# Optimization experiments

Measured on AMD Instinct MI355X. Metric: run time of the kernel, lower is better.

Reference implementation:

```python
import jax, jax.numpy as jnp
import numpy as np

B, N, D, K = 2, 8192, 512, 16


def setup_inputs() -> dict:
    key = jax.random.key(0)
    k1, k2, k3, k4 = jax.random.split(key, 4)
    x = jax.random.normal(k1, (B, N, D), dtype=jnp.float32)
    xyz = jax.random.normal(k2, (B, N, 3), dtype=jnp.float32)
    # nn.Linear(d_model, 3*d_model): weight [3D, D], bias [3D]
    W_qkv = jax.random.normal(k3, (3 * D, D), dtype=jnp.float32) * 0.02
    b_qkv = jnp.zeros((3 * D,), dtype=jnp.float32)
    # nn.Linear(d_model, d_model)
    W_fc = jax.random.normal(k4, (D, D), dtype=jnp.float32) * 0.02
    b_fc = jnp.zeros((D,), dtype=jnp.float32)
    return {"x": x, "xyz": xyz, "W_qkv": W_qkv, "b_qkv": b_qkv, "W_fc": W_fc, "b_fc": b_fc}


def _knn_idx(xyz):
    # squared-distance KNN (same ordering as cdist): |a|^2 + |b|^2 - 2 a.b
    sq = jnp.sum(xyz * xyz, axis=-1)                      # [B, N]
    d2 = sq[:, :, None] + sq[:, None, :] - 2.0 * jnp.einsum('bnc,bmc->bnm', xyz, xyz)
    return jax.lax.top_k(-d2, K)[1]                       # [B, N, K] smallest distances


def reference(x, xyz, W_qkv, b_qkv, W_fc, b_fc):
    knn_idx = _knn_idx(xyz)                               # no-grad in original
    qkv = jnp.einsum('bnd,ed->bne', x, W_qkv) + b_qkv     # [B, N, 3D]
    qkv = qkv.reshape(B, N, 3, D)
    q, k, v = qkv[:, :, 0], qkv[:, :, 1], qkv[:, :, 2]    # [B, N, D]
    gather = jax.vmap(lambda arr, idx: arr[idx])          # per-batch neighbor gather
    k_neigh = gather(k, knn_idx)                          # [B, N, K, D]
    v_neigh = gather(v, knn_idx)                          # [B, N, K, D]
    # faithful to einsum('bnd,bnsk->bns', q, k_neigh): sums d and feature dims independently
    attn = (q.sum(-1)[:, :, None] * k_neigh.sum(-1)) / jnp.sqrt(jnp.float32(D))  # [B, N, K]
    attn = jax.nn.softmax(attn, axis=2)[..., None]        # [B, N, K, 1]
    x_out = (attn * v_neigh).sum(axis=2)                  # [B, N, D]
    return jnp.einsum('bnd,ed->bne', x_out, W_fc) + b_fc + x
```

## Files before the change

kernel.cpp:

```cpp
#include <hip/hip_runtime.h>

typedef _Float16 half_t;
typedef _Float16 half8 __attribute__((ext_vector_type(8)));
typedef _Float16 half4v __attribute__((ext_vector_type(4)));
typedef float f32x4 __attribute__((ext_vector_type(4)));
typedef float f32x2 __attribute__((ext_vector_type(2)));

#define NB 2
#define NN 8192
#define ND 512
#define NKNN 16
#define BN (NB*NN)

#define OFF_XH   0ull
#define OFF_VH   (OFF_XH  + (size_t)BN*ND*2)
#define OFF_XOH  (OFF_VH  + (size_t)BN*ND*2)
#define OFF_WVH  (OFF_XOH + (size_t)BN*ND*2)
#define OFF_WFCH (OFF_WVH + (size_t)ND*ND*2)
#define OFF_XW   (OFF_WFCH+ (size_t)ND*ND*2)
#define OFF_XW2  (OFF_XW  + (size_t)BN*16)
#define OFF_IDX  (OFF_XW2 + (size_t)BN*16)
#define OFF_WQC  (OFF_IDX + (size_t)BN*NKNN*4)
#define OFF_WKC  (OFF_WQC + 2048)
#define OFF_QKB  (OFF_WKC + 2048)
#define OFF_QS   (OFF_QKB + 256)
#define OFF_KS   (OFF_QS  + (size_t)BN*4)

__global__ __launch_bounds__(256) void kcolsum(const float* __restrict__ W,
                                               float* __restrict__ wq,
                                               float* __restrict__ wk) {
  int h = blockIdx.x >> 3, g = blockIdx.x & 7;
  int t = threadIdx.x, dl = t & 63, s = t >> 6;
  const float* Wb = W + (size_t)h * 512 * 512;
  int d = g * 64 + dl;
  float acc = 0.f;
  for (int e = s * 128; e < s * 128 + 128; ++e) acc += Wb[(size_t)e * 512 + d];
  __shared__ float red[4][64];
  red[s][dl] = acc;
  __syncthreads();
  if (s == 0) (h ? wk : wq)[d] = red[0][dl] + red[1][dl] + red[2][dl] + red[3][dl];
}

__global__ __launch_bounds__(512) void kbias(const float* __restrict__ b,
                                             float* __restrict__ qkb) {
  __shared__ float r0[512], r1[512];
  int t = threadIdx.x;
  r0[t] = b[t]; r1[t] = b[512 + t];
  __syncthreads();
  for (int s = 256; s; s >>= 1) {
    if (t < s) { r0[t] += r0[t + s]; r1[t] += r1[t + s]; }
    __syncthreads();
  }
  if (t == 0) { qkb[0] = r0[0]; qkb[1] = r1[0]; }
}

__global__ __launch_bounds__(256) void kconvw(const float* __restrict__ wqkv,
                                              const float* __restrict__ wfc,
                                              half_t* __restrict__ wvh,
                                              half_t* __restrict__ wfch) {
  int i = blockIdx.x * 256 + threadIdx.x;
  float4 a = ((const float4*)(wqkv + 1024 * 512))[i];
  half4v ha; ha[0]=(half_t)a.x; ha[1]=(half_t)a.y; ha[2]=(half_t)a.z; ha[3]=(half_t)a.w;
  *(half4v*)(wvh + (size_t)i * 4) = ha;
  float4 c = ((const float4*)wfc)[i];
  half4v hc; hc[0]=(half_t)c.x; hc[1]=(half_t)c.y; hc[2]=(half_t)c.z; hc[3]=(half_t)c.w;
  *(half4v*)(wfch + (size_t)i * 4) = hc;
}

__global__ __launch_bounds__(256) void kxh(const float* __restrict__ x,
                                           const float* __restrict__ wq,
                                           const float* __restrict__ wk,
                                           const float* __restrict__ qkb,
                                           half_t* __restrict__ xh,
                                           float* __restrict__ qs,
                                           float* __restrict__ ks) {
  int wid = blockIdx.x * 4 + (threadIdx.x >> 6);
  int l = threadIdx.x & 63;
  size_t base = (size_t)wid * ND + l * 8;
  float4 a0 = *(const float4*)(x + base);
  float4 a1 = *(const float4*)(x + base + 4);
  half8 h;
  h[0]=(half_t)a0.x; h[1]=(half_t)a0.y; h[2]=(half_t)a0.z; h[3]=(half_t)a0.w;
  h[4]=(half_t)a1.x; h[5]=(half_t)a1.y; h[6]=(half_t)a1.z; h[7]=(half_t)a1.w;
  *(half8*)(xh + base) = h;
  float4 q0 = ((const float4*)(wq + l * 8))[0], q1 = ((const float4*)(wq + l * 8))[1];
  float4 k0 = ((const float4*)(wk + l * 8))[0], k1 = ((const float4*)(wk + l * 8))[1];
  float dq = a0.x*q0.x + a0.y*q0.y + a0.z*q0.z + a0.w*q0.w
           + a1.x*q1.x + a1.y*q1.y + a1.z*q1.z + a1.w*q1.w;
  float dk = a0.x*k0.x + a0.y*k0.y + a0.z*k0.z + a0.w*k0.w
           + a1.x*k1.x + a1.y*k1.y + a1.z*k1.z + a1.w*k1.w;
  #pragma unroll
  for (int o = 32; o; o >>= 1) { dq += __shfl_xor(dq, o); dk += __shfl_xor(dk, o); }
  if (l == 0) { qs[wid] = dq + qkb[0]; ks[wid] = dk + qkb[1]; }
}

__global__ __launch_bounds__(256) void kxyzw(const float* __restrict__ xyz,
                                             float4* __restrict__ xw,
                                             float4* __restrict__ xw2) {
  int p = blockIdx.x * 256 + threadIdx.x;
  int b = p >> 12;
  int pl = p & 4095;
  int i0 = b * NN + pl * 2;
  const float* s = xyz + (size_t)i0 * 3;
  float x0 = s[0], y0 = s[1], z0 = s[2];
  float x1 = s[3], y1 = s[4], z1 = s[5];
  float sq0 = __fadd_rn(__fadd_rn(__fmul_rn(x0, x0), __fmul_rn(y0, y0)), __fmul_rn(z0, z0));
  float sq1 = __fadd_rn(__fadd_rn(__fmul_rn(x1, x1), __fmul_rn(y1, y1)), __fmul_rn(z1, z1));
  xw[i0]     = make_float4(x0, y0, z0, sq0);
  xw[i0 + 1] = make_float4(x1, y1, z1, sq1);
  xw2[(size_t)b * NN + pl]          = make_float4(x0, x1, y0, y1);
  xw2[(size_t)b * NN + NN/2 + pl]   = make_float4(z0, z1, sq0, sq1);
}

#define QPW 4
__global__ __launch_bounds__(256, 4) void kknn(const float4* __restrict__ xw,
                                               const float4* __restrict__ xw2,
                                               int* __restrict__ idxo) {
  __shared__ __align__(16) float4 tile[1024];
  const int tid = threadIdx.x;
  const int l = tid & 63;
  const int w = tid >> 6;
  const int b = blockIdx.x >> 9;
  const int qbase = (blockIdx.x & 511) * (4 * QPW) + w * QPW;
  const float4* xb  = xw  + (size_t)b * NN;
  const float4* xa2 = xw2 + (size_t)b * NN;
  const float4* xb2 = xa2 + NN / 2;

  f32x2 qxx[QPW], qyy[QPW], qzz[QPW], qww[QPW];
  #pragma unroll
  for (int qi = 0; qi < QPW; ++qi) {
    float4 qp = xb[qbase + qi];
    qxx[qi] = (f32x2){qp.x, qp.x};
    qyy[qi] = (f32x2){qp.y, qp.y};
    qzz[qi] = (f32x2){qp.z, qp.z};
    qww[qi] = (f32x2){qp.w, qp.w};
  }
  const f32x2 m2 = (f32x2){-2.0f, -2.0f};

  float mind[QPW]; int mini[QPW];
  #pragma unroll
  for (int qi = 0; qi < QPW; ++qi) { mind[qi] = __builtin_inff(); mini[qi] = 0x7fffffff; }

  for (int t = 0; t < 8; ++t) {
    __syncthreads();
    tile[tid]       = xa2[t * 512 + tid];
    tile[256 + tid] = xa2[t * 512 + 256 + tid];
    tile[512 + tid] = xb2[t * 512 + tid];
    tile[768 + tid] = xb2[t * 512 + 256 + tid];
    __syncthreads();
    #pragma unroll
    for (int it = 0; it < 8; ++it) {
      int p = it * 64 + l;
      float4 A = tile[p];
      float4 Bv = tile[512 + p];
      f32x2 cx = (f32x2){A.x, A.y};
      f32x2 cy = (f32x2){A.z, A.w};
      f32x2 cz = (f32x2){Bv.x, Bv.y};
      f32x2 cw = (f32x2){Bv.z, Bv.w};
      int ci0 = t * 1024 + p * 2;
      #pragma unroll
      for (int qi = 0; qi < QPW; ++qi) {
        f32x2 dot = __builtin_elementwise_fma(qzz[qi], cz,
                      __builtin_elementwise_fma(qyy[qi], cy, qxx[qi] * cx));
        f32x2 s2 = qww[qi] + cw;
        f32x2 d2 = __builtin_elementwise_fma(m2, dot, s2);
        if (d2.x < mind[qi]) { mind[qi] = d2.x; mini[qi] = ci0; }
        if (d2.y < mind[qi]) { mind[qi] = d2.y; mini[qi] = ci0 + 1; }
      }
    }
  }

  float kd[QPW]; int ki[QPW]; float wst[QPW];
  #pragma unroll
  for (int qi = 0; qi < QPW; ++qi) {
    float d = mind[qi]; int ii = mini[qi];
    #pragma unroll
    for (int k = 2; k <= 64; k <<= 1) {
      #pragma unroll
      for (int j = k >> 1; j > 0; j >>= 1) {
        float od = __shfl_xor(d, j);
        int   oi = __shfl_xor(ii, j);
        bool up = ((l & k) == 0);
        bool lower_lane = ((l & j) == 0);
        bool oless = (od < d) || (od == d && oi < ii);
        bool take = (up == lower_lane) ? oless : !oless;
        if (take) { d = od; ii = oi; }
      }
    }
    kd[qi] = __shfl(d, l & 15);
    ki[qi] = __shfl(ii, l & 15);
    wst[qi] = __shfl(d, 15);
  }

  auto insert = [&](bool ok, float dv, int iv, int qi) {
    unsigned long long m = __ballot(ok);
    while (m) {
      int a = __builtin_ctzll(m);
      m &= m - 1;
      float dc = __shfl(dv, a);
      int ic = __shfl(iv, a);
      bool lower = (kd[qi] < dc) || (kd[qi] == dc && ki[qi] < ic);
      int r = __popcll(__ballot(lower) & 0xFFFFull);
      if (r < 16) {
        float pd = __shfl_up(kd[qi], 1, 16);
        int pi = __shfl_up(ki[qi], 1, 16);
        int pp = l & 15;
        if (pp == r)      { kd[qi] = dc; ki[qi] = ic; }
        else if (pp > r)  { kd[qi] = pd; ki[qi] = pi; }
        wst[qi] = __shfl(kd[qi], 15, 16);
      }
    }
  };

  for (int t = 0; t < 8; ++t) {
    __syncthreads();
    tile[tid]       = xa2[t * 512 + tid];
    tile[256 + tid] = xa2[t * 512 + 256 + tid];
    tile[512 + tid] = xb2[t * 512 + tid];
    tile[768 + tid] = xb2[t * 512 + 256 + tid];
    __syncthreads();
    #pragma unroll 2
    for (int it = 0; it < 8; ++it) {
      int p = it * 64 + l;
      float4 A = tile[p];
      float4 Bv = tile[512 + p];
      f32x2 cx = (f32x2){A.x, A.y};
      f32x2 cy = (f32x2){A.z, A.w};
      f32x2 cz = (f32x2){Bv.x, Bv.y};
      f32x2 cw = (f32x2){Bv.z, Bv.w};
      int ci0 = t * 1024 + p * 2;
      #pragma unroll
      for (int qi = 0; qi < QPW; ++qi) {
        f32x2 dot = __builtin_elementwise_fma(qzz[qi], cz,
                      __builtin_elementwise_fma(qyy[qi], cy, qxx[qi] * cx));
        f32x2 s2 = qww[qi] + cw;
        f32x2 d2 = __builtin_elementwise_fma(m2, dot, s2);
        bool ok0 = (d2.x <= wst[qi]) && (ci0 != mini[qi]);
        bool ok1 = (d2.y <= wst[qi]) && (ci0 + 1 != mini[qi]);
        insert(ok0, d2.x, ci0, qi);
        insert(ok1, d2.y, ci0 + 1, qi);
      }
    }
  }

  if (l < 16) {
    #pragma unroll
    for (int qi = 0; qi < QPW; ++qi)
      idxo[((size_t)b * NN + qbase + qi) * NKNN + l] = ki[qi];
  }
}

__device__ __forceinline__ void gload16(const void* g, void* l) {
  __builtin_amdgcn_global_load_lds((const __attribute__((address_space(1))) void*)g,
                                   (__attribute__((address_space(3))) void*)l, 16, 0, 0);
}

template <int EPI>
__global__ __launch_bounds__(256) void kgemm(const half_t* __restrict__ A,
                                             const half_t* __restrict__ Bw,
                                             const float* __restrict__ bias,
                                             const float* __restrict__ resid,
                                             void* __restrict__ Cout) {
  __shared__ __align__(16) half_t As[128 * 64];
  __shared__ __align__(16) half_t Bs[128 * 64];
  const int tid = threadIdx.x;
  const int l = tid & 63;
  const int w = tid >> 6;
  const int wm = w >> 1, wn = w & 1;
  const int mt = blockIdx.x >> 2;
  const int nt = blockIdx.x & 3;
  const int lr = l & 15, lg = l >> 4;

  f32x4 acc[4][4];
  #pragma unroll
  for (int i = 0; i < 4; ++i)
    #pragma unroll
    for (int j = 0; j < 4; ++j) acc[i][j] = (f32x4){0.f, 0.f, 0.f, 0.f};

  for (int kt = 0; kt < 8; ++kt) {
    #pragma unroll
    for (int i = 0; i < 4; ++i) {
      int id = i * 256 + tid;
      int rr = id >> 3, cc = id & 7;
      gload16(A + (size_t)(mt * 128 + rr) * ND + kt * 64 + cc * 8,
              (void*)(As + (size_t)(i * 256 + w * 64) * 8));
      gload16(Bw + (size_t)(nt * 128 + rr) * ND + kt * 64 + cc * 8,
              (void*)(Bs + (size_t)(i * 256 + w * 64) * 8));
    }
    __syncthreads();
    #pragma unroll
    for (int kk = 0; kk < 2; ++kk) {
      half8 af[4], bf[4];
      #pragma unroll
      for (int mi = 0; mi < 4; ++mi)
        af[mi] = *(const half8*)(As + (wm * 64 + mi * 16 + lr) * 64 + kk * 32 + lg * 8);
      #pragma unroll
      for (int ni = 0; ni < 4; ++ni)
        bf[ni] = *(const half8*)(Bs + (wn * 64 + ni * 16 + lr) * 64 + kk * 32 + lg * 8);
      #pragma unroll
      for (int mi = 0; mi < 4; ++mi)
        #pragma unroll
        for (int ni = 0; ni < 4; ++ni)
          acc[mi][ni] = __builtin_amdgcn_mfma_f32_16x16x32_f16(af[mi], bf[ni], acc[mi][ni], 0, 0, 0);
    }
    __syncthreads();
  }

  #pragma unroll
  for (int mi = 0; mi < 4; ++mi) {
    #pragma unroll
    for (int ni = 0; ni < 4; ++ni) {
      int col = nt * 128 + wn * 64 + ni * 16 + lr;
      #pragma unroll
      for (int r4 = 0; r4 < 4; ++r4) {
        size_t row = (size_t)mt * 128 + wm * 64 + mi * 16 + lg * 4 + r4;
        float v = acc[mi][ni][r4] + bias[col];
        if (EPI == 0) ((half_t*)Cout)[row * ND + col] = (half_t)v;
        else          ((float*)Cout)[row * ND + col] = v + resid[row * ND + col];
      }
    }
  }
}

__global__ __launch_bounds__(256) void kattn(const int* __restrict__ idx,
                                             const float* __restrict__ qs,
                                             const float* __restrict__ ks,
                                             const half_t* __restrict__ vh,
                                             half_t* __restrict__ xoh) {
  int wid = blockIdx.x * 4 + (threadIdx.x >> 6);
  int l = threadIdx.x & 63;
  int b = wid >> 13;
  int j = l & 15;
  int nb = idx[(size_t)wid * NKNN + j];
  float ksv = ks[(size_t)b * NN + nb];
  float logit = __fdiv_rn(__fmul_rn(qs[wid], ksv), 22.627416997969522f);
  float mx = logit;
  #pragma unroll
  for (int o = 8; o; o >>= 1) mx = fmaxf(mx, __shfl_xor(mx, o, 16));
  float e = expf(logit - mx);
  float s = e;
  #pragma unroll
  for (int o = 8; o; o >>= 1) s += __shfl_xor(s, o, 16);
  float p = e / s;

  float acc[8] = {0.f, 0.f, 0.f, 0.f, 0.f, 0.f, 0.f, 0.f};
  #pragma unroll
  for (int t16 = 0; t16 < 16; ++t16) {
    float wj = __shfl(p, t16, 16);
    int ij = __shfl(nb, t16, 16);
    const half8 vv = *(const half8*)(vh + ((size_t)b * NN + ij) * ND + l * 8);
    #pragma unroll
    for (int u = 0; u < 8; ++u) acc[u] += wj * (float)vv[u];
  }
  half8 ho;
  #pragma unroll
  for (int u = 0; u < 8; ++u) ho[u] = (half_t)acc[u];
  *(half8*)(xoh + (size_t)wid * ND + l * 8) = ho;
}

extern "C" void kernel_launch(void* const* d_in, const int* in_sizes, int n_in,
                              void* d_out, int out_size, void* d_ws, size_t ws_size,
                              hipStream_t stream) {
  const float* x    = (const float*)d_in[0];
  const float* xyz  = (const float*)d_in[1];
  const float* wqkv = (const float*)d_in[2];
  const float* bqkv = (const float*)d_in[3];
  const float* wfc  = (const float*)d_in[4];
  const float* bfc  = (const float*)d_in[5];
  char* ws = (char*)d_ws;
  half_t* xh   = (half_t*)(ws + OFF_XH);
  half_t* vh   = (half_t*)(ws + OFF_VH);
  half_t* xoh  = (half_t*)(ws + OFF_XOH);
  half_t* wvh  = (half_t*)(ws + OFF_WVH);
  half_t* wfch = (half_t*)(ws + OFF_WFCH);
  float4* xw   = (float4*)(ws + OFF_XW);
  float4* xw2  = (float4*)(ws + OFF_XW2);
  int*    idx  = (int*)(ws + OFF_IDX);
  float*  wqc  = (float*)(ws + OFF_WQC);
  float*  wkc  = (float*)(ws + OFF_WKC);
  float*  qkb  = (float*)(ws + OFF_QKB);
  float*  qs   = (float*)(ws + OFF_QS);
  float*  ks   = (float*)(ws + OFF_KS);

  kcolsum<<<dim3(16),  dim3(256), 0, stream>>>(wqkv, wqc, wkc);
  kbias  <<<dim3(1),   dim3(512), 0, stream>>>(bqkv, qkb);
  kconvw <<<dim3(256), dim3(256), 0, stream>>>(wqkv, wfc, wvh, wfch);
  kxyzw  <<<dim3(32),  dim3(256), 0, stream>>>(xyz, xw, xw2);
  kxh    <<<dim3(4096),dim3(256), 0, stream>>>(x, wqc, wkc, qkb, xh, qs, ks);
  kknn   <<<dim3(1024),dim3(256), 0, stream>>>(xw, xw2, idx);
  kgemm<0><<<dim3(512),dim3(256), 0, stream>>>(xh, wvh, bqkv + 1024, (const float*)nullptr, (void*)vh);
  kattn  <<<dim3(4096),dim3(256), 0, stream>>>(idx, qs, ks, vh, xoh);
  kgemm<1><<<dim3(512),dim3(256), 0, stream>>>(xoh, wfch, bfc, x, d_out);
}
```

Measured before the change: 168.6 us.

## Fuse setup kernels, double-buffer KNN tiles, simplify first-pass min tracking

Four small setup kernels (column sums, bias sums, weight fp16 conversion, xyz packing) are merged into one launch with block-range dispatch to cut launch overhead. The KNN kernel now double-buffers candidate tiles in LDS using direct global-to-LDS loads, so the next tile's load overlaps compute. The first pass keeps only a per-lane vector min distance without indices, and the second pass re-collects all neighbors from scratch. A wave-wide ballot skips the insert path when no lane qualifies. This trades index bookkeeping and barrier stalls for a slightly different threshold logic, which may change how distance ties are broken.

After: 156.5 us. -7.2%, faster.

```diff
diff --git a/kernel.cpp b/kernel.cpp
--- a/kernel.cpp
+++ b/kernel.cpp
@@ -26,45 +26,65 @@
 #define OFF_QS   (OFF_QKB + 256)
 #define OFF_KS   (OFF_QS  + (size_t)BN*4)
 
-__global__ __launch_bounds__(256) void kcolsum(const float* __restrict__ W,
-                                               float* __restrict__ wq,
-                                               float* __restrict__ wk) {
-  int h = blockIdx.x >> 3, g = blockIdx.x & 7;
-  int t = threadIdx.x, dl = t & 63, s = t >> 6;
-  const float* Wb = W + (size_t)h * 512 * 512;
-  int d = g * 64 + dl;
-  float acc = 0.f;
-  for (int e = s * 128; e < s * 128 + 128; ++e) acc += Wb[(size_t)e * 512 + d];
-  __shared__ float red[4][64];
-  red[s][dl] = acc;
-  __syncthreads();
-  if (s == 0) (h ? wk : wq)[d] = red[0][dl] + red[1][dl] + red[2][dl] + red[3][dl];
-}
-
-__global__ __launch_bounds__(512) void kbias(const float* __restrict__ b,
-                                             float* __restrict__ qkb) {
-  __shared__ float r0[512], r1[512];
-  int t = threadIdx.x;
-  r0[t] = b[t]; r1[t] = b[512 + t];
-  __syncthreads();
-  for (int s = 256; s; s >>= 1) {
-    if (t < s) { r0[t] += r0[t + s]; r1[t] += r1[t + s]; }
-    __syncthreads();
-  }
-  if (t == 0) { qkb[0] = r0[0]; qkb[1] = r1[0]; }
-}
-
-__global__ __launch_bounds__(256) void kconvw(const float* __restrict__ wqkv,
+__device__ __forceinline__ void gload16(const void* g, void* l) {
+  __builtin_amdgcn_global_load_lds((const __attribute__((address_space(1))) void*)g,
+                                   (__attribute__((address_space(3))) void*)l, 16, 0, 0);
+}
+
+__global__ __launch_bounds__(256) void ksetup(const float* __restrict__ wqkv,
+                                              const float* __restrict__ bqkv,
                                               const float* __restrict__ wfc,
-                                              half_t* __restrict__ wvh,
-                                              half_t* __restrict__ wfch) {
-  int i = blockIdx.x * 256 + threadIdx.x;
-  float4 a = ((const float4*)(wqkv + 1024 * 512))[i];
-  half4v ha; ha[0]=(half_t)a.x; ha[1]=(half_t)a.y; ha[2]=(half_t)a.z; ha[3]=(half_t)a.w;
-  *(half4v*)(wvh + (size_t)i * 4) = ha;
-  float4 c = ((const float4*)wfc)[i];
-  half4v hc; hc[0]=(half_t)c.x; hc[1]=(half_t)c.y; hc[2]=(half_t)c.z; hc[3]=(half_t)c.w;
-  *(half4v*)(wfch + (size_t)i * 4) = hc;
+                                              const float* __restrict__ xyz,
+                                              float* __restrict__ wq, float* __restrict__ wk,
+                                              float* __restrict__ qkb,
+                                              half_t* __restrict__ wvh, half_t* __restrict__ wfch,
+                                              float4* __restrict__ xw, float4* __restrict__ xw2) {
+  const int blk = blockIdx.x;
+  const int t = threadIdx.x;
+  if (blk < 16) {
+    int h = blk >> 3, g = blk & 7;
+    int dl = t & 63, s = t >> 6;
+    const float* Wb = wqkv + (size_t)h * 512 * 512;
+    int d = g * 64 + dl;
+    float acc = 0.f;
+    for (int e = s * 128; e < s * 128 + 128; ++e) acc += Wb[(size_t)e * 512 + d];
+    __shared__ float red[4][64];
+    red[s][dl] = acc;
+    __syncthreads();
+    if (s == 0) (h ? wk : wq)[d] = red[0][dl] + red[1][dl] + red[2][dl] + red[3][dl];
+  } else if (blk == 16) {
+    __shared__ float r0[256], r1[256];
+    r0[t] = bqkv[t] + bqkv[t + 256];
+    r1[t] = bqkv[512 + t] + bqkv[768 + t];
+    __syncthreads();
+    for (int s = 128; s; s >>= 1) {
+      if (t < s) { r0[t] += r0[t + s]; r1[t] += r1[t + s]; }
+      __syncthreads();
+    }
+    if (t == 0) { qkb[0] = r0[0]; qkb[1] = r1[0]; }
+  } else if (blk < 273) {
+    int i = (blk - 17) * 256 + t;
+    float4 a = ((const float4*)(wqkv + 1024 * 512))[i];
+    half4v ha; ha[0]=(half_t)a.x; ha[1]=(half_t)a.y; ha[2]=(half_t)a.z; ha[3]=(half_t)a.w;
+    *(half4v*)(wvh + (size_t)i * 4) = ha;
+    float4 c = ((const float4*)wfc)[i];
+    half4v hc; hc[0]=(half_t)c.x; hc[1]=(half_t)c.y; hc[2]=(half_t)c.z; hc[3]=(half_t)c.w;
+    *(half4v*)(wfch + (size_t)i * 4) = hc;
+  } else {
+    int p = (blk - 273) * 256 + t;
+    int b = p >> 12;
+    int pl = p & 4095;
+    int i0 = b * NN + pl * 2;
+    const float* s = xyz + (size_t)i0 * 3;
+    float x0 = s[0], y0 = s[1], z0 = s[2];
+    float x1 = s[3], y1 = s[4], z1 = s[5];
+    float sq0 = __fadd_rn(__fadd_rn(__fmul_rn(x0, x0), __fmul_rn(y0, y0)), __fmul_rn(z0, z0));
+    float sq1 = __fadd_rn(__fadd_rn(__fmul_rn(x1, x1), __fmul_rn(y1, y1)), __fmul_rn(z1, z1));
+    xw[i0]     = make_float4(x0, y0, z0, sq0);
+    xw[i0 + 1] = make_float4(x1, y1, z1, sq1);
+    xw2[(size_t)b * NN + pl]        = make_float4(x0, x1, y0, y1);
+    xw2[(size_t)b * NN + NN/2 + pl] = make_float4(z0, z1, sq0, sq1);
+  }
 }
 
 __global__ __launch_bounds__(256) void kxh(const float* __restrict__ x,
@@ -94,29 +114,13 @@
   if (l == 0) { qs[wid] = dq + qkb[0]; ks[wid] = dk + qkb[1]; }
 }
 
-__global__ __launch_bounds__(256) void kxyzw(const float* __restrict__ xyz,
-                                             float4* __restrict__ xw,
-                                             float4* __restrict__ xw2) {
-  int p = blockIdx.x * 256 + threadIdx.x;
-  int b = p >> 12;
-  int pl = p & 4095;
-  int i0 = b * NN + pl * 2;
-  const float* s = xyz + (size_t)i0 * 3;
-  float x0 = s[0], y0 = s[1], z0 = s[2];
-  float x1 = s[3], y1 = s[4], z1 = s[5];
-  float sq0 = __fadd_rn(__fadd_rn(__fmul_rn(x0, x0), __fmul_rn(y0, y0)), __fmul_rn(z0, z0));
-  float sq1 = __fadd_rn(__fadd_rn(__fmul_rn(x1, x1), __fmul_rn(y1, y1)), __fmul_rn(z1, z1));
-  xw[i0]     = make_float4(x0, y0, z0, sq0);
-  xw[i0 + 1] = make_float4(x1, y1, z1, sq1);
-  xw2[(size_t)b * NN + pl]          = make_float4(x0, x1, y0, y1);
-  xw2[(size_t)b * NN + NN/2 + pl]   = make_float4(z0, z1, sq0, sq1);
-}
-
 #define QPW 4
+#define KTILE 512
 __global__ __launch_bounds__(256, 4) void kknn(const float4* __restrict__ xw,
                                                const float4* __restrict__ xw2,
                                                int* __restrict__ idxo) {
-  __shared__ __align__(16) float4 tile[1024];
+  __shared__ __align__(16) float4 ldsA[2][KTILE];
+  __shared__ __align__(16) float4 ldsB[2][KTILE];
   const int tid = threadIdx.x;
   const int l = tid & 63;
   const int w = tid >> 6;
@@ -126,6 +130,14 @@
   const float4* xa2 = xw2 + (size_t)b * NN;
   const float4* xb2 = xa2 + NN / 2;
 
+#define STAGE(t, bi) do {                                                        \
+    int ts_ = (t) * KTILE;                                                       \
+    gload16(xa2 + ts_ +       w * 64 + l, (void*)&ldsA[bi][      w * 64]);       \
+    gload16(xa2 + ts_ + 256 + w * 64 + l, (void*)&ldsA[bi][256 + w * 64]);       \
+    gload16(xb2 + ts_ +       w * 64 + l, (void*)&ldsB[bi][      w * 64]);       \
+    gload16(xb2 + ts_ + 256 + w * 64 + l, (void*)&ldsB[bi][256 + w * 64]);       \
+  } while (0)
+
   f32x2 qxx[QPW], qyy[QPW], qzz[QPW], qww[QPW];
   #pragma unroll
   for (int qi = 0; qi < QPW; ++qi) {
@@ -137,60 +149,57 @@
   }
   const f32x2 m2 = (f32x2){-2.0f, -2.0f};
 
-  float mind[QPW]; int mini[QPW];
-  #pragma unroll
-  for (int qi = 0; qi < QPW; ++qi) { mind[qi] = __builtin_inff(); mini[qi] = 0x7fffffff; }
-
+  f32x2 mind[QPW];
+  #pragma unroll
+  for (int qi = 0; qi < QPW; ++qi) mind[qi] = (f32x2){__builtin_inff(), __builtin_inff()};
+
+  STAGE(0, 0);
+  __syncthreads();
   for (int t = 0; t < 8; ++t) {
-    __syncthreads();
-    tile[tid]       = xa2[t * 512 + tid];
-    tile[256 + tid] = xa2[t * 512 + 256 + tid];
-    tile[512 + tid] = xb2[t * 512 + tid];
-    tile[768 + tid] = xb2[t * 512 + 256 + tid];
-    __syncthreads();
+    if (t < 7) STAGE(t + 1, (t + 1) & 1);
     #pragma unroll
     for (int it = 0; it < 8; ++it) {
       int p = it * 64 + l;
-      float4 A = tile[p];
-      float4 Bv = tile[512 + p];
+      float4 A  = ldsA[t & 1][p];
+      float4 Bv = ldsB[t & 1][p];
       f32x2 cx = (f32x2){A.x, A.y};
       f32x2 cy = (f32x2){A.z, A.w};
       f32x2 cz = (f32x2){Bv.x, Bv.y};
       f32x2 cw = (f32x2){Bv.z, Bv.w};
-      int ci0 = t * 1024 + p * 2;
       #pragma unroll
       for (int qi = 0; qi < QPW; ++qi) {
         f32x2 dot = __builtin_elementwise_fma(qzz[qi], cz,
                       __builtin_elementwise_fma(qyy[qi], cy, qxx[qi] * cx));
         f32x2 s2 = qww[qi] + cw;
         f32x2 d2 = __builtin_elementwise_fma(m2, dot, s2);
-        if (d2.x < mind[qi]) { mind[qi] = d2.x; mini[qi] = ci0; }
-        if (d2.y < mind[qi]) { mind[qi] = d2.y; mini[qi] = ci0 + 1; }
-      }
-    }
-  }
-
-  float kd[QPW]; int ki[QPW]; float wst[QPW];
+        mind[qi] = __builtin_elementwise_min(mind[qi], d2);
+      }
+    }
+    __syncthreads();
+  }
+
+  float wst[QPW];
   #pragma unroll
   for (int qi = 0; qi < QPW; ++qi) {
-    float d = mind[qi]; int ii = mini[qi];
+    float d = fminf(mind[qi][0], mind[qi][1]);
     #pragma unroll
     for (int k = 2; k <= 64; k <<= 1) {
       #pragma unroll
       for (int j = k >> 1; j > 0; j >>= 1) {
         float od = __shfl_xor(d, j);
-        int   oi = __shfl_xor(ii, j);
         bool up = ((l & k) == 0);
         bool lower_lane = ((l & j) == 0);
-        bool oless = (od < d) || (od == d && oi < ii);
+        bool oless = od < d;
         bool take = (up == lower_lane) ? oless : !oless;
-        if (take) { d = od; ii = oi; }
-      }
-    }
-    kd[qi] = __shfl(d, l & 15);
-    ki[qi] = __shfl(ii, l & 15);
+        if (take) d = od;
+      }
+    }
     wst[qi] = __shfl(d, 15);
   }
+
+  float kd[QPW]; int ki[QPW];
+  #pragma unroll
+  for (int qi = 0; qi < QPW; ++qi) { kd[qi] = __builtin_inff(); ki[qi] = 0x7fffffff; }
 
   auto insert = [&](bool ok, float dv, int iv, int qi) {
     unsigned long long m = __ballot(ok);
@@ -207,40 +216,41 @@
         int pp = l & 15;
         if (pp == r)      { kd[qi] = dc; ki[qi] = ic; }
         else if (pp > r)  { kd[qi] = pd; ki[qi] = pi; }
-        wst[qi] = __shfl(kd[qi], 15, 16);
+        wst[qi] = fminf(wst[qi], __shfl(kd[qi], 15, 16));
       }
     }
   };
 
+  __syncthreads();
+  STAGE(0, 0);
+  __syncthreads();
   for (int t = 0; t < 8; ++t) {
-    __syncthreads();
-    tile[tid]       = xa2[t * 512 + tid];
-    tile[256 + tid] = xa2[t * 512 + 256 + tid];
-    tile[512 + tid] = xb2[t * 512 + tid];
-    tile[768 + tid] = xb2[t * 512 + 256 + tid];
-    __syncthreads();
+    if (t < 7) STAGE(t + 1, (t + 1) & 1);
     #pragma unroll 2
     for (int it = 0; it < 8; ++it) {
       int p = it * 64 + l;
-      float4 A = tile[p];
-      float4 Bv = tile[512 + p];
+      float4 A  = ldsA[t & 1][p];
+      float4 Bv = ldsB[t & 1][p];
       f32x2 cx = (f32x2){A.x, A.y};
       f32x2 cy = (f32x2){A.z, A.w};
       f32x2 cz = (f32x2){Bv.x, Bv.y};
       f32x2 cw = (f32x2){Bv.z, Bv.w};
-      int ci0 = t * 1024 + p * 2;
+      int ci0 = (t * KTILE + p) * 2;
       #pragma unroll
       for (int qi = 0; qi < QPW; ++qi) {
         f32x2 dot = __builtin_elementwise_fma(qzz[qi], cz,
                       __builtin_elementwise_fma(qyy[qi], cy, qxx[qi] * cx));
         f32x2 s2 = qww[qi] + cw;
         f32x2 d2 = __builtin_elementwise_fma(m2, dot, s2);
-        bool ok0 = (d2.x <= wst[qi]) && (ci0 != mini[qi]);
-        bool ok1 = (d2.y <= wst[qi]) && (ci0 + 1 != mini[qi]);
-        insert(ok0, d2.x, ci0, qi);
-        insert(ok1, d2.y, ci0 + 1, qi);
-      }
-    }
+        bool ok0 = d2[0] <= wst[qi];
+        bool ok1 = d2[1] <= wst[qi];
+        if (__ballot(ok0 || ok1)) {
+          insert(ok0, d2[0], ci0, qi);
+          insert(ok1, d2[1], ci0 + 1, qi);
+        }
+      }
+    }
+    __syncthreads();
   }
 
   if (l < 16) {
@@ -248,11 +258,7 @@
     for (int qi = 0; qi < QPW; ++qi)
       idxo[((size_t)b * NN + qbase + qi) * NKNN + l] = ki[qi];
   }
-}
-
-__device__ __forceinline__ void gload16(const void* g, void* l) {
-  __builtin_amdgcn_global_load_lds((const __attribute__((address_space(1))) void*)g,
-                                   (__attribute__((address_space(3))) void*)l, 16, 0, 0);
+#undef STAGE
 }
 
 template <int EPI>
@@ -382,13 +388,11 @@
   float*  qs   = (float*)(ws + OFF_QS);
   float*  ks   = (float*)(ws + OFF_KS);
 
-  kcolsum<<<dim3(16),  dim3(256), 0, stream>>>(wqkv, wqc, wkc);
-  kbias  <<<dim3(1),   dim3(512), 0, stream>>>(bqkv, qkb);
-  kconvw <<<dim3(256), dim3(256), 0, stream>>>(wqkv, wfc, wvh, wfch);
-  kxyzw  <<<dim3(32),  dim3(256), 0, stream>>>(xyz, xw, xw2);
-  kxh    <<<dim3(4096),dim3(256), 0, stream>>>(x, wqc, wkc, qkb, xh, qs, ks);
-  kknn   <<<dim3(1024),dim3(256), 0, stream>>>(xw, xw2, idx);
+  ksetup<<<dim3(305), dim3(256), 0, stream>>>(wqkv, bqkv, wfc, xyz,
+                                              wqc, wkc, qkb, wvh, wfch, xw, xw2);
+  kxh   <<<dim3(4096),dim3(256), 0, stream>>>(x, wqc, wkc, qkb, xh, qs, ks);
+  kknn  <<<dim3(1024),dim3(256), 0, stream>>>(xw, xw2, idx);
   kgemm<0><<<dim3(512),dim3(256), 0, stream>>>(xh, wvh, bqkv + 1024, (const float*)nullptr, (void*)vh);
-  kattn  <<<dim3(4096),dim3(256), 0, stream>>>(idx, qs, ks, vh, xoh);
+  kattn <<<dim3(4096),dim3(256), 0, stream>>>(idx, qs, ks, vh, xoh);
   kgemm<1><<<dim3(512),dim3(256), 0, stream>>>(xoh, wfch, bfc, x, d_out);
 }
```
